# Optimization experiments

Measured on AMD Instinct MI355X. Metric: run time of the kernel, lower is better.

The kernel has to match this reference:

```python
import jax, jax.numpy as jnp
import numpy as np

N_NODES = 100000
N_EDGES = 1600000
IN_FEATS = 128
H1 = 256
H2 = 256
N_CLASSES = 64


def setup_inputs() -> dict:
    key = jax.random.key(0)
    ks = jax.random.split(key, 12)
    x = jax.random.normal(ks[0], (N_NODES, IN_FEATS), dtype=jnp.float32)
    src = jax.random.randint(ks[1], (N_EDGES,), 0, N_NODES, dtype=jnp.int64 if jax.config.jax_enable_x64 else jnp.int32)
    dst = jax.random.randint(ks[2], (N_EDGES,), 0, N_NODES, dtype=jnp.int64 if jax.config.jax_enable_x64 else jnp.int32)
    def lin(kw, kb, fan_in, fan_out):
        bound = 1.0 / np.sqrt(fan_in)
        W = jax.random.uniform(kw, (fan_out, fan_in), minval=-bound, maxval=bound, dtype=jnp.float32)
        b = jax.random.uniform(kb, (fan_out,), minval=-bound, maxval=bound, dtype=jnp.float32)
        return W, b
    W1, b1 = lin(ks[3], ks[4], 2 * IN_FEATS, H1)
    W2, b2 = lin(ks[5], ks[6], 2 * H1, H2)
    W3, b3 = lin(ks[7], ks[8], 2 * H2, N_CLASSES)
    return {"x": x, "src": src, "dst": dst,
            "W1": W1, "b1": b1, "W2": W2, "b2": b2, "W3": W3, "b3": b3}


def _sage_conv(h, src, dst, W, b):
    # message = copy from src node, reduce = mean at dst node (DGL copy_u + mean)
    m = jnp.take(h, src, axis=0)                                  # [E, d]
    s = jax.ops.segment_sum(m, dst, num_segments=N_NODES)         # [N, d]
    deg = jax.ops.segment_sum(jnp.ones((m.shape[0],), h.dtype), dst,
                              num_segments=N_NODES)               # [N]
    h_N = s / jnp.maximum(deg, 1.0)[:, None]                      # isolated nodes -> 0 (DGL behavior)
    h_total = jnp.concatenate([h, h_N], axis=1)                   # [N, 2d]
    return h_total @ W.T + b                                      # dropout inactive at eval (p=0.05)


def reference(x, src, dst, W1, b1, W2, b2, W3, b3):
    h = jax.nn.relu(_sage_conv(x, src, dst, W1, b1))
    h = jax.nn.relu(_sage_conv(h, src, dst, W2, b2))
    return _sage_conv(h, src, dst, W3, b3)
```

## Files before the change

### kernel.cpp

```cpp
#include <hip/hip_runtime.h>
#include <hip/hip_bf16.h>
#include <cstdint>
#include <cstddef>

#define N_NODES 100000
#define N_EDGES 1600000
#define NBUCK   128
#define NPB     782
#define NB_E    ((N_EDGES + 4095) / 4096)

typedef __attribute__((ext_vector_type(8))) short short8;
typedef __attribute__((ext_vector_type(4))) float floatx4;

__device__ inline float bf_lo(unsigned int u) { return __uint_as_float(u << 16); }
__device__ inline float bf_hi(unsigned int u) { return __uint_as_float(u & 0xffff0000u); }
__device__ inline unsigned short f2bf(float f) {
  unsigned int u = __float_as_uint(f);
  u += 0x7fffu + ((u >> 16) & 1u);
  return (unsigned short)(u >> 16);
}

__global__ void cvt_f32_bf16(const float* __restrict__ in,
                             unsigned short* __restrict__ out, int n4) {
  int t = blockIdx.x * blockDim.x + threadIdx.x;
  if (t >= n4) return;
  float4 v = ((const float4*)in)[t];
  ushort4 o;
  o.x = f2bf(v.x); o.y = f2bf(v.y); o.z = f2bf(v.z); o.w = f2bf(v.w);
  ((ushort4*)out)[t] = o;
}

__global__ void cvt_w3cat(const float* __restrict__ W3, unsigned short* __restrict__ out) {
  int t = blockIdx.x * blockDim.x + threadIdx.x;
  if (t >= 128 * 256 / 4) return;
  int idx4 = t * 4;
  int r = idx4 >> 8, c = idx4 & 255;
  float4 v = *(const float4*)(W3 + (size_t)(r & 63) * 512 + (r >> 6) * 256 + c);
  ushort4 o;
  o.x = f2bf(v.x); o.y = f2bf(v.y); o.z = f2bf(v.z); o.w = f2bf(v.w);
  *(ushort4*)(out + (size_t)r * 256 + c) = o;
}

__device__ inline int wave_incl_scan(int v, int lane) {
#pragma unroll
  for (int off = 1; off < 64; off <<= 1) {
    int t = __shfl_up(v, off, 64);
    if (lane >= off) v += t;
  }
  return v;
}

__global__ __launch_bounds__(256)
void pass1a_kernel(const int* __restrict__ dst, int* __restrict__ bucketCount) {
  __shared__ int hist[NBUCK];
  if (threadIdx.x < NBUCK) hist[threadIdx.x] = 0;
  __syncthreads();
#pragma unroll
  for (int i = 0; i < 16; ++i) {
    int e = blockIdx.x * 4096 + i * 256 + threadIdx.x;
    if (e < N_EDGES) atomicAdd(&hist[dst[e] / NPB], 1);
  }
  __syncthreads();
  if (threadIdx.x < NBUCK) atomicAdd(&bucketCount[threadIdx.x], hist[threadIdx.x]);
}

__global__ void scanB_kernel(const int* __restrict__ bucketCount,
                             int* __restrict__ bucketBase, int* __restrict__ gCursorB) {
  __shared__ int wsum[2];
  int t = threadIdx.x, lane = t & 63, wid = t >> 6;
  int v = bucketCount[t];
  int incl = wave_incl_scan(v, lane);
  if (lane == 63) wsum[wid] = incl;
  __syncthreads();
  int off = (wid == 1) ? wsum[0] : 0;
  bucketBase[t] = off + incl - v;
  gCursorB[t]   = off + incl - v;
  if (t == 127) bucketBase[NBUCK] = off + incl;
}

__global__ __launch_bounds__(256)
void pass1b_kernel(const int* __restrict__ src, const int* __restrict__ dst,
                   int* __restrict__ gCursorB, unsigned int* __restrict__ staging) {
  __shared__ int hist[NBUCK];
  if (threadIdx.x < NBUCK) hist[threadIdx.x] = 0;
  __syncthreads();
#pragma unroll
  for (int i = 0; i < 16; ++i) {
    int e = blockIdx.x * 4096 + i * 256 + threadIdx.x;
    if (e < N_EDGES) atomicAdd(&hist[dst[e] / NPB], 1);
  }
  __syncthreads();
  if (threadIdx.x < NBUCK)
    hist[threadIdx.x] = atomicAdd(&gCursorB[threadIdx.x], hist[threadIdx.x]);
  __syncthreads();
#pragma unroll
  for (int i = 0; i < 16; ++i) {
    int e = blockIdx.x * 4096 + i * 256 + threadIdx.x;
    if (e < N_EDGES) {
      int d = dst[e];
      int b = d / NPB;
      int pos = atomicAdd(&hist[b], 1);
      staging[pos] = (unsigned)src[e] | ((unsigned)(d - b * NPB) << 17);
    }
  }
}

__global__ __launch_bounds__(1024)
void pass2_kernel(const unsigned int* __restrict__ staging, const int* __restrict__ bucketBase,
                  int* __restrict__ start, float* __restrict__ invdeg,
                  int* __restrict__ esrc) {
  __shared__ int cnt[1024];
  __shared__ int cur[1024];
  __shared__ int wsum[16];
  const int b = blockIdx.x, tid = threadIdx.x;
  const int lane = tid & 63, wid = tid >> 6;
  const int n0 = b * NPB, n1 = min(n0 + NPB, N_NODES);
  const int nLocal = n1 - n0;
  const int p0 = bucketBase[b], p1 = bucketBase[b + 1];

  cnt[tid] = 0;
  __syncthreads();
  for (int e = p0 + tid; e < p1; e += 1024)
    atomicAdd(&cnt[staging[e] >> 17], 1);
  __syncthreads();

  int c = cnt[tid];
  int incl = wave_incl_scan(c, lane);
  if (lane == 63) wsum[wid] = incl;
  __syncthreads();
  if (wid == 0) {
    int v = (lane < 16) ? wsum[lane] : 0;
    int i2 = wave_incl_scan(v, lane);
    if (lane < 16) wsum[lane] = i2 - v;
  }
  __syncthreads();
  int excl = wsum[wid] + incl - c;
  cur[tid] = excl;
  if (tid < nLocal) {
    start[n0 + tid] = p0 + excl;
    invdeg[n0 + tid] = 1.0f / fmaxf((float)c, 1.0f);
  }
  if (b == NBUCK - 1 && tid == 0) start[N_NODES] = N_EDGES;
  __syncthreads();

  for (int e = p0 + tid; e < p1; e += 1024) {
    unsigned int pr = staging[e];
    int pos = p0 + atomicAdd(&cur[pr >> 17], 1);
    esrc[pos] = (int)(pr & 0x1FFFFu);
  }
}

template<int D>
__global__ __launch_bounds__(256)
void gather_mean(const unsigned short* __restrict__ h,
                 const int* __restrict__ start,
                 const int* __restrict__ esrc,
                 const float* __restrict__ invdeg,
                 unsigned short* __restrict__ hn) {
  int wave = (int)((blockIdx.x * 256 + threadIdx.x) >> 6);
  if (wave >= N_NODES) return;
  int lane = threadIdx.x & 63;
  int s0 = start[wave], s1 = start[wave + 1];
  constexpr int FPL = D / 64;
  float acc[FPL] = {};
  const unsigned short* base = h + lane * FPL;

  int e = s0;
  if constexpr (FPL == 4) {
    for (; e + 4 <= s1; e += 4) {
      int sn0 = esrc[e], sn1 = esrc[e + 1], sn2 = esrc[e + 2], sn3 = esrc[e + 3];
      uint2 p0 = *(const uint2*)(base + (size_t)sn0 * D);
      uint2 p1 = *(const uint2*)(base + (size_t)sn1 * D);
      uint2 p2 = *(const uint2*)(base + (size_t)sn2 * D);
      uint2 p3 = *(const uint2*)(base + (size_t)sn3 * D);
      acc[0] += bf_lo(p0.x) + bf_lo(p1.x) + bf_lo(p2.x) + bf_lo(p3.x);
      acc[1] += bf_hi(p0.x) + bf_hi(p1.x) + bf_hi(p2.x) + bf_hi(p3.x);
      acc[2] += bf_lo(p0.y) + bf_lo(p1.y) + bf_lo(p2.y) + bf_lo(p3.y);
      acc[3] += bf_hi(p0.y) + bf_hi(p1.y) + bf_hi(p2.y) + bf_hi(p3.y);
    }
    for (; e < s1; ++e) {
      int sn = esrc[e];
      uint2 p = *(const uint2*)(base + (size_t)sn * D);
      acc[0] += bf_lo(p.x); acc[1] += bf_hi(p.x);
      acc[2] += bf_lo(p.y); acc[3] += bf_hi(p.y);
    }
  } else {
    for (; e + 4 <= s1; e += 4) {
      int sn0 = esrc[e], sn1 = esrc[e + 1], sn2 = esrc[e + 2], sn3 = esrc[e + 3];
      unsigned int p0 = *(const unsigned int*)(base + (size_t)sn0 * D);
      unsigned int p1 = *(const unsigned int*)(base + (size_t)sn1 * D);
      unsigned int p2 = *(const unsigned int*)(base + (size_t)sn2 * D);
      unsigned int p3 = *(const unsigned int*)(base + (size_t)sn3 * D);
      acc[0] += bf_lo(p0) + bf_lo(p1) + bf_lo(p2) + bf_lo(p3);
      acc[1] += bf_hi(p0) + bf_hi(p1) + bf_hi(p2) + bf_hi(p3);
    }
    for (; e < s1; ++e) {
      int sn = esrc[e];
      unsigned int p = *(const unsigned int*)(base + (size_t)sn * D);
      acc[0] += bf_lo(p); acc[1] += bf_hi(p);
    }
  }

  float inv = invdeg[wave];
  unsigned short* out = hn + (size_t)wave * D + lane * FPL;
  if constexpr (FPL == 4) {
    ushort4 o;
    o.x = f2bf(acc[0] * inv); o.y = f2bf(acc[1] * inv);
    o.z = f2bf(acc[2] * inv); o.w = f2bf(acc[3] * inv);
    *(ushort4*)out = o;
  } else {
    ushort2 o;
    o.x = f2bf(acc[0] * inv); o.y = f2bf(acc[1] * inv);
    *(ushort2*)out = o;
  }
}

__global__ __launch_bounds__(256)
void gather_add64(const unsigned short* __restrict__ Y3,
                  const int* __restrict__ start, const int* __restrict__ esrc,
                  const float* __restrict__ invdeg, float* __restrict__ out) {
  int wave = (int)((blockIdx.x * 256 + threadIdx.x) >> 6);
  if (wave >= N_NODES) return;
  int lane = threadIdx.x & 63;
  int half = lane >> 5, l32 = lane & 31;
  int s0 = start[wave], s1 = start[wave + 1];
  float a0 = 0.f, a1 = 0.f;
  for (int e = s0 + half; e < s1; e += 2) {
    int sn = esrc[e];
    unsigned int p = *(const unsigned int*)(Y3 + (size_t)sn * 64 + 2 * l32);
    a0 += bf_lo(p); a1 += bf_hi(p);
  }
  a0 += __shfl_xor(a0, 32, 64);
  a1 += __shfl_xor(a1, 32, 64);
  if (half == 0) {
    float inv = invdeg[wave];
    float2* q = (float2*)(out + (size_t)wave * 64 + 2 * l32);
    float2 v = *q;
    v.x += inv * a0; v.y += inv * a1;
    *q = v;
  }
}

template<int D, int DOUT, int BN, bool RELU, bool OUTF32, int MODE>
__global__ __launch_bounds__(256)
void sage_gemm(const unsigned short* __restrict__ H,
               const unsigned short* __restrict__ HN,
               const unsigned short* __restrict__ Wb,
               const float* __restrict__ bias,
               void* __restrict__ outp,
               unsigned short* __restrict__ y3) {
  constexpr int K   = (MODE == 1) ? D : 2 * D;
  constexpr int BM  = 128, KC = 32;
  constexpr int NCHUNK = K / KC;
  constexpr int AF  = BM / 16;
  constexpr int BF  = BN / 16;
  constexpr int FR  = AF + BF;
  constexpr int NMF = 4;
  constexpr int NJF = BF / 2;

  __shared__ __align__(16) unsigned short lds0[FR * 512];
  __shared__ __align__(16) unsigned short lds1[FR * 512];

  const int tid  = threadIdx.x;
  const int wave = tid >> 6, lane = tid & 63;
  const int l16  = lane & 15, quad = lane >> 4;
  const int n0   = blockIdx.x * BM;
  const int bn0  = blockIdx.y * BN;
  const int wm   = wave >> 1, wn = wave & 1;

  floatx4 acc[NMF][NJF] = {};

  auto stage = [&](int c, unsigned short* buf) {
    const int kc = c * KC;
    const unsigned short* srcH = (kc < D) ? H : HN;
    const int kb = (kc < D) ? kc : kc - D;
    const int w0 = __builtin_amdgcn_readfirstlane(wave);
#pragma unroll
    for (int i = 0; i < FR / 4; ++i) {
      const int fu = w0 + 4 * i;
      const unsigned short* g;
      if (fu < AF) {
        int row = min(n0 + fu * 16 + l16, N_NODES - 1);
        g = srcH + (size_t)row * D + kb + quad * 8;
      } else {
        int col = bn0 + (fu - AF) * 16 + l16;
        g = Wb + (size_t)col * K + kc + quad * 8;
      }
      __builtin_amdgcn_global_load_lds(
          (const __attribute__((address_space(1))) unsigned int*)g,
          (__attribute__((address_space(3))) unsigned int*)(buf + fu * 512),
          16, 0, 0);
    }
  };

  auto compute = [&](const unsigned short* buf) {
    short8 b[NJF];
#pragma unroll
    for (int jt = 0; jt < NJF; ++jt)
      b[jt] = *(const short8*)(buf + (AF + wn * NJF + jt) * 512 + lane * 8);
#pragma unroll
    for (int mi = 0; mi < NMF; ++mi) {
      short8 a = *(const short8*)(buf + (wm * NMF + mi) * 512 + lane * 8);
#pragma unroll
      for (int jt = 0; jt < NJF; ++jt)
        acc[mi][jt] = __builtin_amdgcn_mfma_f32_16x16x32_bf16(a, b[jt], acc[mi][jt], 0, 0, 0);
    }
  };

  stage(0, lds0);
  __syncthreads();
#pragma unroll 1
  for (int c = 0; c < NCHUNK; c += 2) {
    stage(c + 1, lds1);
    compute(lds0);
    __syncthreads();
    if (c + 2 < NCHUNK) stage(c + 2, lds0);
    compute(lds1);
    __syncthreads();
  }

#pragma unroll
  for (int mi = 0; mi < NMF; ++mi) {
#pragma unroll
    for (int jt = 0; jt < NJF; ++jt) {
      int j = bn0 + wn * (NJF * 16) + jt * 16 + l16;
      float bj = (MODE == 1 && wn == 1) ? 0.0f : bias[j];
#pragma unroll
      for (int r = 0; r < 4; ++r) {
        int node = n0 + wm * 64 + mi * 16 + quad * 4 + r;
        if (node < N_NODES) {
          float v = acc[mi][jt][r];
          if constexpr (MODE == 1) {
            if (wn == 0) ((float*)outp)[(size_t)node * 64 + j] = v + bj;
            else y3[(size_t)node * 64 + (j - 64)] = f2bf(v);
          } else {
            v += bj;
            if (RELU) v = fmaxf(v, 0.0f);
            if (OUTF32) ((float*)outp)[(size_t)node * DOUT + j] = v;
            else ((unsigned short*)outp)[(size_t)node * DOUT + j] = f2bf(v);
          }
        }
      }
    }
  }
}

extern "C" void kernel_launch(void* const* d_in, const int* in_sizes, int n_in,
                              void* d_out, int out_size, void* d_ws, size_t ws_size,
                              hipStream_t stream) {
  const float* x   = (const float*)d_in[0];
  const int*   src = (const int*)d_in[1];
  const int*   dst = (const int*)d_in[2];
  const float* W1 = (const float*)d_in[3];
  const float* b1 = (const float*)d_in[4];
  const float* W2 = (const float*)d_in[5];
  const float* b2 = (const float*)d_in[6];
  const float* W3 = (const float*)d_in[7];
  const float* b3 = (const float*)d_in[8];

  char* ws = (char*)d_ws;
  unsigned short* H0 = (unsigned short*)ws; ws += (size_t)N_NODES * 128 * 2;
  unsigned short* H1 = (unsigned short*)ws; ws += (size_t)N_NODES * 256 * 2;
  unsigned short* H2 = (unsigned short*)ws; ws += (size_t)N_NODES * 256 * 2;
  unsigned short* HN = (unsigned short*)ws; ws += (size_t)N_NODES * 256 * 2;
  unsigned int* staging = (unsigned int*)ws; ws += (size_t)N_EDGES * 4;
  int* esrc   = (int*)ws;  ws += (size_t)N_EDGES * 4;
  int* startp = (int*)ws;  ws += (size_t)(N_NODES + 32) * 4;
  float* invdeg = (float*)ws; ws += (size_t)(N_NODES + 32) * 4;
  int* bucketCount = (int*)ws; ws += 512;
  int* bucketBase  = (int*)ws; ws += 1024;
  int* gCursorB    = (int*)ws; ws += 512;
  unsigned short* Y3 = (unsigned short*)ws; ws += (size_t)N_NODES * 64 * 2;
  unsigned short* Wb1 = (unsigned short*)ws; ws += 256 * 256 * 2;
  unsigned short* Wb2 = (unsigned short*)ws; ws += 256 * 512 * 2;
  unsigned short* Wb3 = (unsigned short*)ws; ws += 128 * 256 * 2;

  hipMemsetAsync(bucketCount, 0, NBUCK * 4, stream);
  pass1a_kernel<<<NB_E, 256, 0, stream>>>(dst, bucketCount);
  scanB_kernel<<<1, 128, 0, stream>>>(bucketCount, bucketBase, gCursorB);
  pass1b_kernel<<<NB_E, 256, 0, stream>>>(src, dst, gCursorB, staging);
  pass2_kernel<<<NBUCK, 1024, 0, stream>>>(staging, bucketBase, startp, invdeg, esrc);

  cvt_f32_bf16<<<(N_NODES * 128 / 4 + 255) / 256, 256, 0, stream>>>(x, H0, N_NODES * 128 / 4);
  cvt_f32_bf16<<<(256 * 256 / 4 + 255) / 256, 256, 0, stream>>>(W1, Wb1, 256 * 256 / 4);
  cvt_f32_bf16<<<(256 * 512 / 4 + 255) / 256, 256, 0, stream>>>(W2, Wb2, 256 * 512 / 4);
  cvt_w3cat<<<(128 * 256 / 4 + 255) / 256, 256, 0, stream>>>(W3, Wb3);

  const int GGRID = (N_NODES * 64 + 255) / 256;
  const int MG = (N_NODES + 127) / 128;

  gather_mean<128><<<GGRID, 256, 0, stream>>>(H0, startp, esrc, invdeg, HN);
  sage_gemm<128, 256, 128, true, false, 0><<<dim3(MG, 2), 256, 0, stream>>>(H0, HN, Wb1, b1, H1, nullptr);

  gather_mean<256><<<GGRID, 256, 0, stream>>>(H1, startp, esrc, invdeg, HN);
  sage_gemm<256, 256, 128, true, false, 0><<<dim3(MG, 2), 256, 0, stream>>>(H1, HN, Wb2, b2, H2, nullptr);

  sage_gemm<256, 128, 128, false, true, 1><<<dim3(MG, 1), 256, 0, stream>>>(H2, nullptr, Wb3, b3, (float*)d_out, Y3);
  gather_add64<<<GGRID, 256, 0, stream>>>(Y3, startp, esrc, invdeg, (float*)d_out);
}
```

Measured before the change: 616.4 us.

## Use full-width GEMM tiles and split layer-2 gather across column halves

The SAGE GEMMs now cover the whole output width in one block (BM=64, BN=256 for layers 1-2), so each block reads its node rows once instead of once per column block, and the wave layout is generalized. The 256-wide gather is split into two column-half grid slices, each lane loading 4 bytes per edge instead of 8. This trades the redundant A-tile loads for fewer rows per block. The split gather doubles the start/esrc index reads and loses the wider per-lane loads.

```diff
diff --git a/kernel.cpp b/kernel.cpp
--- a/kernel.cpp
+++ b/kernel.cpp
@@ -150,69 +150,44 @@
   }
 }
 
-template<int D>
+template<int D, int SPLIT>
 __global__ __launch_bounds__(256)
 void gather_mean(const unsigned short* __restrict__ h,
                  const int* __restrict__ start,
                  const int* __restrict__ esrc,
                  const float* __restrict__ invdeg,
                  unsigned short* __restrict__ hn) {
+  constexpr int CW = D / SPLIT;
+  constexpr int FPL = CW / 64;
   int wave = (int)((blockIdx.x * 256 + threadIdx.x) >> 6);
   if (wave >= N_NODES) return;
   int lane = threadIdx.x & 63;
+  int colbase = blockIdx.y * CW;
   int s0 = start[wave], s1 = start[wave + 1];
-  constexpr int FPL = D / 64;
-  float acc[FPL] = {};
-  const unsigned short* base = h + lane * FPL;
+  float acc0 = 0.f, acc1 = 0.f;
+  const unsigned short* base = h + colbase + lane * FPL;
 
   int e = s0;
-  if constexpr (FPL == 4) {
-    for (; e + 4 <= s1; e += 4) {
-      int sn0 = esrc[e], sn1 = esrc[e + 1], sn2 = esrc[e + 2], sn3 = esrc[e + 3];
-      uint2 p0 = *(const uint2*)(base + (size_t)sn0 * D);
-      uint2 p1 = *(const uint2*)(base + (size_t)sn1 * D);
-      uint2 p2 = *(const uint2*)(base + (size_t)sn2 * D);
-      uint2 p3 = *(const uint2*)(base + (size_t)sn3 * D);
-      acc[0] += bf_lo(p0.x) + bf_lo(p1.x) + bf_lo(p2.x) + bf_lo(p3.x);
-      acc[1] += bf_hi(p0.x) + bf_hi(p1.x) + bf_hi(p2.x) + bf_hi(p3.x);
-      acc[2] += bf_lo(p0.y) + bf_lo(p1.y) + bf_lo(p2.y) + bf_lo(p3.y);
-      acc[3] += bf_hi(p0.y) + bf_hi(p1.y) + bf_hi(p2.y) + bf_hi(p3.y);
-    }
-    for (; e < s1; ++e) {
-      int sn = esrc[e];
-      uint2 p = *(const uint2*)(base + (size_t)sn * D);
-      acc[0] += bf_lo(p.x); acc[1] += bf_hi(p.x);
-      acc[2] += bf_lo(p.y); acc[3] += bf_hi(p.y);
-    }
-  } else {
-    for (; e + 4 <= s1; e += 4) {
-      int sn0 = esrc[e], sn1 = esrc[e + 1], sn2 = esrc[e + 2], sn3 = esrc[e + 3];
-      unsigned int p0 = *(const unsigned int*)(base + (size_t)sn0 * D);
-      unsigned int p1 = *(const unsigned int*)(base + (size_t)sn1 * D);
-      unsigned int p2 = *(const unsigned int*)(base + (size_t)sn2 * D);
-      unsigned int p3 = *(const unsigned int*)(base + (size_t)sn3 * D);
-      acc[0] += bf_lo(p0) + bf_lo(p1) + bf_lo(p2) + bf_lo(p3);
-      acc[1] += bf_hi(p0) + bf_hi(p1) + bf_hi(p2) + bf_hi(p3);
-    }
-    for (; e < s1; ++e) {
-      int sn = esrc[e];
-      unsigned int p = *(const unsigned int*)(base + (size_t)sn * D);
-      acc[0] += bf_lo(p); acc[1] += bf_hi(p);
-    }
+  for (; e + 4 <= s1; e += 4) {
+    int sn0 = esrc[e], sn1 = esrc[e + 1], sn2 = esrc[e + 2], sn3 = esrc[e + 3];
+    unsigned int p0 = *(const unsigned int*)(base + (size_t)sn0 * D);
+    unsigned int p1 = *(const unsigned int*)(base + (size_t)sn1 * D);
+    unsigned int p2 = *(const unsigned int*)(base + (size_t)sn2 * D);
+    unsigned int p3 = *(const unsigned int*)(base + (size_t)sn3 * D);
+    acc0 += bf_lo(p0) + bf_lo(p1) + bf_lo(p2) + bf_lo(p3);
+    acc1 += bf_hi(p0) + bf_hi(p1) + bf_hi(p2) + bf_hi(p3);
+  }
+  for (; e < s1; ++e) {
+    int sn = esrc[e];
+    unsigned int p = *(const unsigned int*)(base + (size_t)sn * D);
+    acc0 += bf_lo(p); acc1 += bf_hi(p);
   }
 
   float inv = invdeg[wave];
-  unsigned short* out = hn + (size_t)wave * D + lane * FPL;
-  if constexpr (FPL == 4) {
-    ushort4 o;
-    o.x = f2bf(acc[0] * inv); o.y = f2bf(acc[1] * inv);
-    o.z = f2bf(acc[2] * inv); o.w = f2bf(acc[3] * inv);
-    *(ushort4*)out = o;
-  } else {
-    ushort2 o;
-    o.x = f2bf(acc[0] * inv); o.y = f2bf(acc[1] * inv);
-    *(ushort2*)out = o;
-  }
+  unsigned short* out = hn + (size_t)wave * D + colbase + lane * FPL;
+  ushort2 o;
+  o.x = f2bf(acc0 * inv); o.y = f2bf(acc1 * inv);
+  *(ushort2*)out = o;
 }
 
 __global__ __launch_bounds__(256)
@@ -241,7 +216,7 @@
   }
 }
 
-template<int D, int DOUT, int BN, bool RELU, bool OUTF32, int MODE>
+template<int D, int DOUT, int BM, int BN, bool RELU, bool OUTF32, int MODE>
 __global__ __launch_bounds__(256)
 void sage_gemm(const unsigned short* __restrict__ H,
                const unsigned short* __restrict__ HN,
@@ -250,13 +225,15 @@
                void* __restrict__ outp,
                unsigned short* __restrict__ y3) {
   constexpr int K   = (MODE == 1) ? D : 2 * D;
-  constexpr int BM  = 128, KC = 32;
+  constexpr int KC  = 32;
   constexpr int NCHUNK = K / KC;
   constexpr int AF  = BM / 16;
   constexpr int BF  = BN / 16;
   constexpr int FR  = AF + BF;
-  constexpr int NMF = 4;
-  constexpr int NJF = BF / 2;
+  constexpr int WAVES_N = BN / 64;
+  constexpr int WAVES_M = 4 / WAVES_N;
+  constexpr int NMF = BM / (16 * WAVES_M);
+  constexpr int NJF = 4;
 
   __shared__ __align__(16) unsigned short lds0[FR * 512];
   __shared__ __align__(16) unsigned short lds1[FR * 512];
@@ -265,8 +242,7 @@
   const int wave = tid >> 6, lane = tid & 63;
   const int l16  = lane & 15, quad = lane >> 4;
   const int n0   = blockIdx.x * BM;
-  const int bn0  = blockIdx.y * BN;
-  const int wm   = wave >> 1, wn = wave & 1;
+  const int wm   = wave / WAVES_N, wn = wave % WAVES_N;
 
   floatx4 acc[NMF][NJF] = {};
 
@@ -283,7 +259,7 @@
         int row = min(n0 + fu * 16 + l16, N_NODES - 1);
         g = srcH + (size_t)row * D + kb + quad * 8;
       } else {
-        int col = bn0 + (fu - AF) * 16 + l16;
+        int col = (fu - AF) * 16 + l16;
         g = Wb + (size_t)col * K + kc + quad * 8;
       }
       __builtin_amdgcn_global_load_lds(
@@ -323,15 +299,15 @@
   for (int mi = 0; mi < NMF; ++mi) {
 #pragma unroll
     for (int jt = 0; jt < NJF; ++jt) {
-      int j = bn0 + wn * (NJF * 16) + jt * 16 + l16;
-      float bj = (MODE == 1 && wn == 1) ? 0.0f : bias[j];
+      int j = wn * 64 + jt * 16 + l16;
+      float bj = (MODE == 1 && j >= 64) ? 0.0f : bias[MODE == 1 ? (j & 63) : j];
 #pragma unroll
       for (int r = 0; r < 4; ++r) {
-        int node = n0 + wm * 64 + mi * 16 + quad * 4 + r;
+        int node = n0 + wm * (NMF * 16) + mi * 16 + quad * 4 + r;
         if (node < N_NODES) {
           float v = acc[mi][jt][r];
           if constexpr (MODE == 1) {
-            if (wn == 0) ((float*)outp)[(size_t)node * 64 + j] = v + bj;
+            if (j < 64) ((float*)outp)[(size_t)node * 64 + j] = v + bj;
             else y3[(size_t)node * 64 + (j - 64)] = f2bf(v);
           } else {
             v += bj;
@@ -387,14 +363,15 @@
   cvt_w3cat<<<(128 * 256 / 4 + 255) / 256, 256, 0, stream>>>(W3, Wb3);
 
   const int GGRID = (N_NODES * 64 + 255) / 256;
-  const int MG = (N_NODES + 127) / 128;
-
-  gather_mean<128><<<GGRID, 256, 0, stream>>>(H0, startp, esrc, invdeg, HN);
-  sage_gemm<128, 256, 128, true, false, 0><<<dim3(MG, 2), 256, 0, stream>>>(H0, HN, Wb1, b1, H1, nullptr);
-
-  gather_mean<256><<<GGRID, 256, 0, stream>>>(H1, startp, esrc, invdeg, HN);
-  sage_gemm<256, 256, 128, true, false, 0><<<dim3(MG, 2), 256, 0, stream>>>(H1, HN, Wb2, b2, H2, nullptr);
-
-  sage_gemm<256, 128, 128, false, true, 1><<<dim3(MG, 1), 256, 0, stream>>>(H2, nullptr, Wb3, b3, (float*)d_out, Y3);
+  const int MG64  = (N_NODES + 63) / 64;
+  const int MG128 = (N_NODES + 127) / 128;
+
+  gather_mean<128, 1><<<dim3(GGRID, 1), 256, 0, stream>>>(H0, startp, esrc, invdeg, HN);
+  sage_gemm<128, 256, 64, 256, true, false, 0><<<MG64, 256, 0, stream>>>(H0, HN, Wb1, b1, H1, nullptr);
+
+  gather_mean<256, 2><<<dim3(GGRID, 2), 256, 0, stream>>>(H1, startp, esrc, invdeg, HN);
+  sage_gemm<256, 256, 64, 256, true, false, 0><<<MG64, 256, 0, stream>>>(H1, HN, Wb2, b2, H2, nullptr);
+
+  sage_gemm<256, 128, 128, 128, false, true, 1><<<MG128, 256, 0, stream>>>(H2, nullptr, Wb3, b3, (float*)d_out, Y3);
   gather_add64<<<GGRID, 256, 0, stream>>>(Y3, startp, esrc, invdeg, (float*)d_out);
 }
```

Measured after the change: 652.3 us. 1.06x slower.
